# Kernel optimization log

Hardware: AMD Instinct MI355X
Metric: run time of the kernel (lower is better)

## Reference

```python
import jax, jax.numpy as jnp
import numpy as np


def setup_inputs() -> dict:
    key = jax.random.key(0)
    k1, k2, k3, k4 = jax.random.split(key, 4)
    B, S, H, U, C = 64, 512, 768, 16, 5
    hidden = jax.random.normal(k1, (B, S, H), dtype=jnp.float32)
    # per-token utterance index, sorted so each utterance is a contiguous span
    segment_ids = jnp.sort(jax.random.randint(k2, (B, S), 0, U), axis=-1).astype(jnp.int32)
    W_h = jax.random.normal(k3, (H, H), dtype=jnp.float32) * 0.02
    b_h = jnp.zeros((H,), dtype=jnp.float32)
    W_o = jax.random.normal(k4, (H, C), dtype=jnp.float32) * 0.02
    b_o = jnp.zeros((C,), dtype=jnp.float32)
    return {"hidden": hidden, "segment_ids": segment_ids, "n_utter": U,
            "W_h": W_h, "b_h": b_h, "W_o": W_o, "b_o": b_o}


def reference(hidden, segment_ids, n_utter, W_h, b_h, W_o, b_o):
    # hidden: [B,S,H]; segment_ids: [B,S] in [0, n_utter)
    B, S, H = hidden.shape
    n_segments = B * n_utter
    # globalize segment ids across the batch
    flat_seg = (segment_ids + jnp.arange(B, dtype=segment_ids.dtype)[:, None] * n_utter).reshape(-1)
    flat_h = hidden.reshape(B * S, H)
    # ragged per-utterance mean via one segment reduce (replaces python slice loop)
    sums = jax.ops.segment_sum(flat_h, flat_seg, num_segments=n_segments)
    counts = jax.ops.segment_sum(jnp.ones((B * S,), dtype=hidden.dtype), flat_seg,
                                 num_segments=n_segments)
    means = sums / jnp.maximum(counts, 1.0)[:, None]  # [B*n_utter, H]
    # linear_h -> SELU -> (dropout is identity in eval) -> linear_o -> softmax
    h = jax.nn.selu(means @ W_h + b_h)
    logits = h @ W_o + b_o
    return jax.nn.softmax(logits, axis=1)
```

## Files before the change

kernel.cpp:

```cpp
#include <hip/hip_runtime.h>
#include <math.h>

#define B 64
#define S 512
#define H 768
#define U 16
#define C 5
#define M (B*U)

typedef __attribute__((ext_vector_type(8))) short short8;
typedef __attribute__((ext_vector_type(4))) float floatx4;

__device__ inline unsigned short f2bf(float x) {
    unsigned u = __float_as_uint(x);
    u += 0x7FFFu + ((u >> 16) & 1u);
    return (unsigned short)(u >> 16);
}
__device__ inline void acc4(float4& a, const float4& v) {
    a.x += v.x; a.y += v.y; a.z += v.z; a.w += v.w;
}

__global__ __launch_bounds__(192) void seg_mean_kernel(
    const float* __restrict__ hidden, const int* __restrict__ seg,
    unsigned short* __restrict__ means)
{
    const int b = blockIdx.x >> 4;
    const int u = blockIdx.x & 15;
    const int* srow = seg + b * S;

    int lo = 0, hi = S;
    while (lo < hi) { int mid = (lo + hi) >> 1; if (srow[mid] < u) lo = mid + 1; else hi = mid; }
    const int start = lo;
    hi = S;
    while (lo < hi) { int mid = (lo + hi) >> 1; if (srow[mid] < u + 1) lo = mid + 1; else hi = mid; }
    const int end = lo;

    const int t = threadIdx.x;
    const float4* h4 = (const float4*)(hidden + (size_t)b * S * H) + t;
    const int ldr = H / 4;

    float4 a0 = make_float4(0.f,0.f,0.f,0.f), a1 = a0, a2 = a0, a3 = a0;
    int s = start;
    #pragma unroll 2
    for (; s + 4 <= end; s += 4) {
        float4 v0 = h4[(size_t)(s + 0) * ldr];
        float4 v1 = h4[(size_t)(s + 1) * ldr];
        float4 v2 = h4[(size_t)(s + 2) * ldr];
        float4 v3 = h4[(size_t)(s + 3) * ldr];
        acc4(a0, v0); acc4(a1, v1); acc4(a2, v2); acc4(a3, v3);
    }
    for (; s < end; ++s) acc4(a0, h4[(size_t)s * ldr]);

    acc4(a0, a1); acc4(a2, a3); acc4(a0, a2);
    const float inv = 1.0f / fmaxf((float)(end - start), 1.0f);
    ushort4 o;
    o.x = f2bf(a0.x * inv); o.y = f2bf(a0.y * inv);
    o.z = f2bf(a0.z * inv); o.w = f2bf(a0.w * inv);
    ((ushort4*)(means + (size_t)(b * U + u) * H))[t] = o;
}

__global__ __launch_bounds__(256) void wh_transpose_kernel(
    const float* __restrict__ Wh, unsigned short* __restrict__ Bt)
{
    __shared__ float tile[32][33];
    const int bn = blockIdx.x % (H / 32);
    const int bk = blockIdx.x / (H / 32);
    const int tx = threadIdx.x & 31;
    const int ty = threadIdx.x >> 5;
    #pragma unroll
    for (int i = 0; i < 4; ++i)
        tile[ty + 8 * i][tx] = Wh[(size_t)(bk * 32 + ty + 8 * i) * H + bn * 32 + tx];
    __syncthreads();
    #pragma unroll
    for (int i = 0; i < 4; ++i)
        Bt[(size_t)(bn * 32 + ty + 8 * i) * H + bk * 32 + tx] = f2bf(tile[tx][ty + 8 * i]);
}

__global__ __launch_bounds__(256) void gemm1_mfma_kernel(
    const unsigned short* __restrict__ means, const unsigned short* __restrict__ Bt,
    const float* __restrict__ bh, float* __restrict__ hout)
{
    const int wid  = threadIdx.x >> 6;
    const int lane = threadIdx.x & 63;
    const int tile = blockIdx.x * 4 + wid;
    const int tm = tile / (H / 32);
    const int tn = tile % (H / 32);
    const int m0 = tm * 16, n0 = tn * 32;

    const int quad = lane >> 4;
    const int l16  = lane & 15;

    const short8* ap  = (const short8*)(means + (size_t)(m0 + l16) * H);
    const short8* bp0 = (const short8*)(Bt    + (size_t)(n0 + l16) * H);
    const short8* bp1 = (const short8*)(Bt    + (size_t)(n0 + 16 + l16) * H);

    floatx4 acc0 = {0.f, 0.f, 0.f, 0.f}, acc1 = acc0;
    #pragma unroll 4
    for (int kk = 0; kk < H / 32; ++kk) {
        short8 a  = ap [4 * kk + quad];
        short8 b0 = bp0[4 * kk + quad];
        short8 b1 = bp1[4 * kk + quad];
        acc0 = __builtin_amdgcn_mfma_f32_16x16x32_bf16(a, b0, acc0, 0, 0, 0);
        acc1 = __builtin_amdgcn_mfma_f32_16x16x32_bf16(a, b1, acc1, 0, 0, 0);
    }

    const float SC = 1.0507009873554805f, AL = 1.6732632423543772f;
    const float bs0 = bh[n0 + l16], bs1 = bh[n0 + 16 + l16];
    #pragma unroll
    for (int r = 0; r < 4; ++r) {
        float* row = hout + (size_t)(m0 + quad * 4 + r) * H;
        float x0 = acc0[r] + bs0;
        float x1 = acc1[r] + bs1;
        row[n0 + l16]      = x0 > 0.f ? SC * x0 : SC * AL * (expf(x0) - 1.f);
        row[n0 + 16 + l16] = x1 > 0.f ? SC * x1 : SC * AL * (expf(x1) - 1.f);
    }
}

__global__ __launch_bounds__(256) void head_kernel(
    const float* __restrict__ hbuf, const float* __restrict__ Wo,
    const float* __restrict__ bo, float* __restrict__ out)
{
    const int wave = threadIdx.x >> 6;
    const int lane = threadIdx.x & 63;
    const int row  = blockIdx.x * 4 + wave;

    float acc[C] = {};
    #pragma unroll
    for (int j = 0; j < H / 64; ++j) {
        int k = lane + 64 * j;
        float hv = hbuf[(size_t)row * H + k];
        #pragma unroll
        for (int cc = 0; cc < C; ++cc) acc[cc] += hv * Wo[k * C + cc];
    }
    #pragma unroll
    for (int off = 32; off >= 1; off >>= 1)
        #pragma unroll
        for (int cc = 0; cc < C; ++cc) acc[cc] += __shfl_down(acc[cc], off);

    if (lane == 0) {
        float l[C], mx = -1e30f;
        #pragma unroll
        for (int cc = 0; cc < C; ++cc) { l[cc] = acc[cc] + bo[cc]; mx = fmaxf(mx, l[cc]); }
        float sum = 0.f;
        #pragma unroll
        for (int cc = 0; cc < C; ++cc) { l[cc] = expf(l[cc] - mx); sum += l[cc]; }
        float r = 1.0f / sum;
        #pragma unroll
        for (int cc = 0; cc < C; ++cc) out[(size_t)row * C + cc] = l[cc] * r;
    }
}

extern "C" void kernel_launch(void* const* d_in, const int* in_sizes, int n_in,
                              void* d_out, int out_size, void* d_ws, size_t ws_size,
                              hipStream_t stream)
{
    const float* hidden = (const float*)d_in[0];
    const int*   seg    = (const int*)d_in[1];
    const float* Wh = (const float*)d_in[3];
    const float* bh = (const float*)d_in[4];
    const float* Wo = (const float*)d_in[5];
    const float* bo = (const float*)d_in[6];
    float* out = (float*)d_out;

    float*          hbuf  = (float*)d_ws;
    unsigned short* means = (unsigned short*)(hbuf + (size_t)M * H);
    unsigned short* Bt    = means + (size_t)M * H;

    wh_transpose_kernel<<<(H / 32) * (H / 32), 256, 0, stream>>>(Wh, Bt);
    seg_mean_kernel<<<M, 192, 0, stream>>>(hidden, seg, means);
    gemm1_mfma_kernel<<<(M / 16) * (H / 32) / 4, 256, 0, stream>>>(means, Bt, bh, hbuf);
    head_kernel<<<M / 4, 256, 0, stream>>>(hbuf, Wo, bo, out);
}
```

Baseline: 187.6 us.

## Fuse head projection into GEMM epilogue and merge prep kernels

Merges the segment-mean and W_h transpose kernels into one launch and also zeroes a logits buffer there. The GEMM epilogue now multiplies its SELU outputs by W_o, reduces across 16 lanes and atomically adds partial logits, so the [M,H] hidden buffer is no longer written and re-read. A small softmax kernel finishes. This removes one launch and the intermediate round trip, at the cost of atomics, which make the summation order nondeterministic.

```diff
diff --git a/kernel.cpp b/kernel.cpp
--- a/kernel.cpp
+++ b/kernel.cpp
@@ -20,65 +20,81 @@
     a.x += v.x; a.y += v.y; a.z += v.z; a.w += v.w;
 }
 
-__global__ __launch_bounds__(192) void seg_mean_kernel(
+__global__ __launch_bounds__(192) void prep_kernel(
     const float* __restrict__ hidden, const int* __restrict__ seg,
-    unsigned short* __restrict__ means)
+    const float* __restrict__ Wh,
+    unsigned short* __restrict__ means, unsigned short* __restrict__ Bt,
+    float* __restrict__ logits)
 {
-    const int b = blockIdx.x >> 4;
-    const int u = blockIdx.x & 15;
-    const int* srow = seg + b * S;
+    __shared__ float tile[32][33];
+    const int t = threadIdx.x;
 
-    int lo = 0, hi = S;
-    while (lo < hi) { int mid = (lo + hi) >> 1; if (srow[mid] < u) lo = mid + 1; else hi = mid; }
-    const int start = lo;
-    hi = S;
-    while (lo < hi) { int mid = (lo + hi) >> 1; if (srow[mid] < u + 1) lo = mid + 1; else hi = mid; }
-    const int end = lo;
+    if (blockIdx.x < M) {
+        const int b = blockIdx.x >> 4;
+        const int u = blockIdx.x & 15;
+        const int* srow = seg + b * S;
 
-    const int t = threadIdx.x;
-    const float4* h4 = (const float4*)(hidden + (size_t)b * S * H) + t;
-    const int ldr = H / 4;
+        int lo = 0, hi = S;
+        while (lo < hi) { int mid = (lo + hi) >> 1; if (srow[mid] < u) lo = mid + 1; else hi = mid; }
+        const int start = lo;
+        hi = S;
+        while (lo < hi) { int mid = (lo + hi) >> 1; if (srow[mid] < u + 1) lo = mid + 1; else hi = mid; }
+        const int end = lo;
 
-    float4 a0 = make_float4(0.f,0.f,0.f,0.f), a1 = a0, a2 = a0, a3 = a0;
-    int s = start;
-    #pragma unroll 2
-    for (; s + 4 <= end; s += 4) {
-        float4 v0 = h4[(size_t)(s + 0) * ldr];
-        float4 v1 = h4[(size_t)(s + 1) * ldr];
-        float4 v2 = h4[(size_t)(s + 2) * ldr];
-        float4 v3 = h4[(size_t)(s + 3) * ldr];
-        acc4(a0, v0); acc4(a1, v1); acc4(a2, v2); acc4(a3, v3);
+        const float4* h4 = (const float4*)(hidden + (size_t)b * S * H) + t;
+        const int ldr = H / 4;
+
+        float4 a0 = make_float4(0.f,0.f,0.f,0.f), a1 = a0, a2 = a0, a3 = a0;
+        int s = start;
+        #pragma unroll 2
+        for (; s + 4 <= end; s += 4) {
+            float4 v0 = h4[(size_t)(s + 0) * ldr];
+            float4 v1 = h4[(size_t)(s + 1) * ldr];
+            float4 v2 = h4[(size_t)(s + 2) * ldr];
+            float4 v3 = h4[(size_t)(s + 3) * ldr];
+            acc4(a0, v0); acc4(a1, v1); acc4(a2, v2); acc4(a3, v3);
+        }
+        for (; s < end; ++s) acc4(a0, h4[(size_t)s * ldr]);
+
+        acc4(a0, a1); acc4(a2, a3); acc4(a0, a2);
+        const float inv = 1.0f / fmaxf((float)(end - start), 1.0f);
+        ushort4 o;
+        o.x = f2bf(a0.x * inv); o.y = f2bf(a0.y * inv);
+        o.z = f2bf(a0.z * inv); o.w = f2bf(a0.w * inv);
+        ((ushort4*)(means + (size_t)(b * U + u) * H))[t] = o;
+        return;
     }
-    for (; s < end; ++s) acc4(a0, h4[(size_t)s * ldr]);
 
-    acc4(a0, a1); acc4(a2, a3); acc4(a0, a2);
-    const float inv = 1.0f / fmaxf((float)(end - start), 1.0f);
-    ushort4 o;
-    o.x = f2bf(a0.x * inv); o.y = f2bf(a0.y * inv);
-    o.z = f2bf(a0.z * inv); o.w = f2bf(a0.w * inv);
-    ((ushort4*)(means + (size_t)(b * U + u) * H))[t] = o;
+    const int tb = blockIdx.x - M;
+    if (tb < 27) {
+        int i = tb * 192 + t;
+        if (i < M * C) logits[i] = 0.f;
+    }
+    const int bn = tb % (H / 32);
+    const int bk = tb / (H / 32);
+    #pragma unroll
+    for (int i = 0; i < 6; ++i) {
+        int idx = t + 192 * i;
+        if (idx < 1024) {
+            int r = idx >> 5, c = idx & 31;
+            tile[r][c] = Wh[(size_t)(bk * 32 + r) * H + bn * 32 + c];
+        }
+    }
+    __syncthreads();
+    #pragma unroll
+    for (int i = 0; i < 6; ++i) {
+        int idx = t + 192 * i;
+        if (idx < 1024) {
+            int r = idx >> 5, c = idx & 31;
+            Bt[(size_t)(bn * 32 + r) * H + bk * 32 + c] = f2bf(tile[c][r]);
+        }
+    }
 }
 
-__global__ __launch_bounds__(256) void wh_transpose_kernel(
-    const float* __restrict__ Wh, unsigned short* __restrict__ Bt)
-{
-    __shared__ float tile[32][33];
-    const int bn = blockIdx.x % (H / 32);
-    const int bk = blockIdx.x / (H / 32);
-    const int tx = threadIdx.x & 31;
-    const int ty = threadIdx.x >> 5;
-    #pragma unroll
-    for (int i = 0; i < 4; ++i)
-        tile[ty + 8 * i][tx] = Wh[(size_t)(bk * 32 + ty + 8 * i) * H + bn * 32 + tx];
-    __syncthreads();
-    #pragma unroll
-    for (int i = 0; i < 4; ++i)
-        Bt[(size_t)(bn * 32 + ty + 8 * i) * H + bk * 32 + tx] = f2bf(tile[tx][ty + 8 * i]);
-}
-
-__global__ __launch_bounds__(256) void gemm1_mfma_kernel(
+__global__ __launch_bounds__(256) void gemm1_fused_kernel(
     const unsigned short* __restrict__ means, const unsigned short* __restrict__ Bt,
-    const float* __restrict__ bh, float* __restrict__ hout)
+    const float* __restrict__ bh, const float* __restrict__ Wo,
+    float* __restrict__ logits)
 {
     const int wid  = threadIdx.x >> 6;
     const int lane = threadIdx.x & 63;
@@ -106,48 +122,48 @@
 
     const float SC = 1.0507009873554805f, AL = 1.6732632423543772f;
     const float bs0 = bh[n0 + l16], bs1 = bh[n0 + 16 + l16];
+    float wo0[C], wo1[C];
+    #pragma unroll
+    for (int c = 0; c < C; ++c) {
+        wo0[c] = Wo[(size_t)(n0 + l16) * C + c];
+        wo1[c] = Wo[(size_t)(n0 + 16 + l16) * C + c];
+    }
+
     #pragma unroll
     for (int r = 0; r < 4; ++r) {
-        float* row = hout + (size_t)(m0 + quad * 4 + r) * H;
         float x0 = acc0[r] + bs0;
         float x1 = acc1[r] + bs1;
-        row[n0 + l16]      = x0 > 0.f ? SC * x0 : SC * AL * (expf(x0) - 1.f);
-        row[n0 + 16 + l16] = x1 > 0.f ? SC * x1 : SC * AL * (expf(x1) - 1.f);
+        float y0 = x0 > 0.f ? SC * x0 : SC * AL * (expf(x0) - 1.f);
+        float y1 = x1 > 0.f ? SC * x1 : SC * AL * (expf(x1) - 1.f);
+        float p[C];
+        #pragma unroll
+        for (int c = 0; c < C; ++c) p[c] = y0 * wo0[c] + y1 * wo1[c];
+        #pragma unroll
+        for (int off = 1; off < 16; off <<= 1)
+            #pragma unroll
+            for (int c = 0; c < C; ++c) p[c] += __shfl_xor(p[c], off);
+        if (l16 == 0) {
+            float* dst = logits + (size_t)(m0 + quad * 4 + r) * C;
+            #pragma unroll
+            for (int c = 0; c < C; ++c) atomicAdd(dst + c, p[c]);
+        }
     }
 }
 
-__global__ __launch_bounds__(256) void head_kernel(
-    const float* __restrict__ hbuf, const float* __restrict__ Wo,
-    const float* __restrict__ bo, float* __restrict__ out)
+__global__ __launch_bounds__(256) void softmax_kernel(
+    const float* __restrict__ logits, const float* __restrict__ bo,
+    float* __restrict__ out)
 {
-    const int wave = threadIdx.x >> 6;
-    const int lane = threadIdx.x & 63;
-    const int row  = blockIdx.x * 4 + wave;
-
-    float acc[C] = {};
+    const int row = blockIdx.x * 256 + threadIdx.x;
+    float l[C], mx = -1e30f;
     #pragma unroll
-    for (int j = 0; j < H / 64; ++j) {
-        int k = lane + 64 * j;
-        float hv = hbuf[(size_t)row * H + k];
-        #pragma unroll
-        for (int cc = 0; cc < C; ++cc) acc[cc] += hv * Wo[k * C + cc];
-    }
+    for (int c = 0; c < C; ++c) { l[c] = logits[(size_t)row * C + c] + bo[c]; mx = fmaxf(mx, l[c]); }
+    float sum = 0.f;
     #pragma unroll
-    for (int off = 32; off >= 1; off >>= 1)
-        #pragma unroll
-        for (int cc = 0; cc < C; ++cc) acc[cc] += __shfl_down(acc[cc], off);
-
-    if (lane == 0) {
-        float l[C], mx = -1e30f;
-        #pragma unroll
-        for (int cc = 0; cc < C; ++cc) { l[cc] = acc[cc] + bo[cc]; mx = fmaxf(mx, l[cc]); }
-        float sum = 0.f;
-        #pragma unroll
-        for (int cc = 0; cc < C; ++cc) { l[cc] = expf(l[cc] - mx); sum += l[cc]; }
-        float r = 1.0f / sum;
-        #pragma unroll
-        for (int cc = 0; cc < C; ++cc) out[(size_t)row * C + cc] = l[cc] * r;
-    }
+    for (int c = 0; c < C; ++c) { l[c] = expf(l[c] - mx); sum += l[c]; }
+    const float rs = 1.0f / sum;
+    #pragma unroll
+    for (int c = 0; c < C; ++c) out[(size_t)row * C + c] = l[c] * rs;
 }
 
 extern "C" void kernel_launch(void* const* d_in, const int* in_sizes, int n_in,
@@ -162,12 +178,11 @@
     const float* bo = (const float*)d_in[6];
     float* out = (float*)d_out;
 
-    float*          hbuf  = (float*)d_ws;
-    unsigned short* means = (unsigned short*)(hbuf + (size_t)M * H);
-    unsigned short* Bt    = means + (size_t)M * H;
+    unsigned short* means  = (unsigned short*)d_ws;
+    unsigned short* Bt     = means + (size_t)M * H;
+    float*          logits = (float*)(Bt + (size_t)H * H);
 
-    wh_transpose_kernel<<<(H / 32) * (H / 32), 256, 0, stream>>>(Wh, Bt);
-    seg_mean_kernel<<<M, 192, 0, stream>>>(hidden, seg, means);
-    gemm1_mfma_kernel<<<(M / 16) * (H / 32) / 4, 256, 0, stream>>>(means, Bt, bh, hbuf);
-    head_kernel<<<M / 4, 256, 0, stream>>>(hbuf, Wo, bo, out);
+    prep_kernel<<<M + (H / 32) * (H / 32), 192, 0, stream>>>(hidden, seg, Wh, means, Bt, logits);
+    gemm1_fused_kernel<<<(M / 16) * (H / 32) / 4, 256, 0, stream>>>(means, Bt, bh, Wo, logits);
+    softmax_kernel<<<M / 256, 256, 0, stream>>>(logits, bo, out);
 }
```

Measured after the change: 198.4 us. 1.06x slower.
